# Kernel optimization log

Hardware: AMD Instinct MI355X
Metric: run time of the kernel (lower is better)

Reference implementation:

```python
import jax, jax.numpy as jnp
import numpy as np

B, S, HID, HEADS = 1, 2048, 4096, 32
HEAD_D = HID // HEADS
SCALE = float(1.0 / np.sqrt(HEAD_D))  # = 1/norm_factor^2 with use_mup=False


def setup_inputs() -> dict:
    key = jax.random.key(0)
    k0, k1, k2, k3, k4 = jax.random.split(key, 5)
    return {
        "x": jax.random.normal(k0, (B, S, HID), jnp.float32),
        "attn_qkvw": jax.random.normal(k1, (HID, 3 * HID), jnp.float32) * 0.02,
        "attn_qkvb": jax.random.normal(k2, (3 * HID,), jnp.float32) * 0.02,
        "attn_ow": jax.random.normal(k3, (HID, HID), jnp.float32) * 0.02,
        "attn_ob": jax.random.normal(k4, (HID,), jnp.float32) * 0.02,
    }


def reference(x, attn_qkvw, attn_qkvb, attn_ow, attn_ob):
    # QKV projection (LinearOp): [B,S,HID] @ [HID,3*HID] + bias -> packed qkv
    qkv = x @ attn_qkvw + attn_qkvb
    q, k, v = jnp.split(qkv, 3, axis=-1)  # each [B,S,HID]

    def to_heads(t):
        return t.reshape(B, S, HEADS, HEAD_D)

    q, k, v = to_heads(q), to_heads(k), to_heads(v)
    # flash kernel math: softmax(scale * q k^T + causal mask) @ v (numerically
    # stable online softmax == standard stable softmax)
    scores = jnp.einsum("bqhd,bkhd->bhqk", q, k) * jnp.float32(SCALE)
    causal = jnp.tril(jnp.ones((S, S), dtype=bool))  # P_SEQ = 0
    scores = jnp.where(causal[None, None], scores, jnp.float32(-jnp.inf))
    attn = jax.nn.softmax(scores, axis=-1)
    ctx = jnp.einsum("bhqk,bkhd->bqhd", attn, v).reshape(B, S, HID)
    # output projection
    return ctx @ attn_ow + attn_ob
```

## Files before the change

### kernel.cpp

```cpp
#include <hip/hip_runtime.h>
#include <hip/hip_bf16.h>
#include <math.h>

typedef __bf16 bf16_t;
typedef __bf16 bf16x8 __attribute__((ext_vector_type(8)));
typedef float f32x4 __attribute__((ext_vector_type(4)));

#define AS1 __attribute__((address_space(1)))
#define AS3 __attribute__((address_space(3)))

static constexpr int S_  = 2048;
static constexpr int HID = 4096;
static constexpr int NH  = 32;
static constexpr int HD  = 128;
static constexpr int N3  = 3 * HID;
static constexpr float SCALE = 0.08838834764831845f;

__global__ void cvt_f32_bf16(const float* __restrict__ in, bf16_t* __restrict__ out, int n4) {
  int i = blockIdx.x * blockDim.x + threadIdx.x;
  if (i >= n4) return;
  float4 v = ((const float4*)in)[i];
  union { bf16_t h[4]; short4 s4; } u;
  u.h[0] = (bf16_t)v.x; u.h[1] = (bf16_t)v.y; u.h[2] = (bf16_t)v.z; u.h[3] = (bf16_t)v.w;
  ((short4*)out)[i] = u.s4;
}

__global__ __launch_bounds__(256) void transcvt64(
    const float* __restrict__ in, bf16_t* __restrict__ out, int R, int C) {
  __shared__ float t[64][65];
  const int r0 = blockIdx.y * 64, c0 = blockIdx.x * 64;
  const int tid = threadIdx.x;
  const int rr = tid >> 4, c4 = (tid & 15) * 4;
#pragma unroll
  for (int it = 0; it < 4; ++it) {
    float4 v = *(const float4*)&in[(size_t)(r0 + rr + it * 16) * C + c0 + c4];
    t[rr + it * 16][c4 + 0] = v.x;
    t[rr + it * 16][c4 + 1] = v.y;
    t[rr + it * 16][c4 + 2] = v.z;
    t[rr + it * 16][c4 + 3] = v.w;
  }
  __syncthreads();
  const int cc = tid >> 3, r8 = (tid & 7) * 8;
#pragma unroll
  for (int it = 0; it < 2; ++it) {
    const int c = cc + it * 32;
    bf16x8 w;
#pragma unroll
    for (int j = 0; j < 8; ++j) w[j] = (bf16_t)t[r8 + j][c];
    *(bf16x8*)&out[(size_t)(c0 + c) * R + r0 + r8] = w;
  }
}

__global__ void vtrans(const bf16_t* __restrict__ qkv, bf16_t* __restrict__ vt) {
  __shared__ bf16_t t[32][33];
  int h = blockIdx.z;
  int s0 = blockIdx.x * 32, d0 = blockIdx.y * 32;
  int tx = threadIdx.x, ty = threadIdx.y;
#pragma unroll
  for (int i = 0; i < 32; i += 8)
    t[ty + i][tx] = qkv[(size_t)(s0 + ty + i) * N3 + 2 * HID + h * HD + d0 + tx];
  __syncthreads();
#pragma unroll
  for (int i = 0; i < 32; i += 8)
    vt[(size_t)(h * HD + d0 + ty + i) * S_ + s0 + tx] = t[tx][ty + i];
}

template <bool STG, int VMC>
__device__ __forceinline__ void wstep(
    const char* slot, int aoff, int boff,
    const bf16_t* gA, const bf16_t* gB, int kst, size_t row64,
    char* stgA, char* stgB, f32x4 (&acc)[8][4]) {
  bf16x8 a[8], b[4];
#pragma unroll
  for (int mi = 0; mi < 8; ++mi) a[mi] = *(const bf16x8*)(slot + aoff + mi * 1024);
#pragma unroll
  for (int ni = 0; ni < 4; ++ni) b[ni] = *(const bf16x8*)(slot + 16384 + boff + ni * 1024);
  if constexpr (STG) {
#pragma unroll
    for (int i = 0; i < 4; ++i)
      __builtin_amdgcn_global_load_lds((const AS1 void*)(gA + i * row64 + kst),
                                       (AS3 void*)(stgA + i * 4096), 16, 0, 0);
#pragma unroll
    for (int j = 0; j < 2; ++j)
      __builtin_amdgcn_global_load_lds((const AS1 void*)(gB + j * row64 + kst),
                                       (AS3 void*)(stgB + j * 4096), 16, 0, 0);
  }
  if constexpr (VMC == 6)      asm volatile("s_waitcnt vmcnt(6)" ::: "memory");
  else if constexpr (VMC == 0) asm volatile("s_waitcnt vmcnt(0)" ::: "memory");
  asm volatile("s_waitcnt lgkmcnt(0)" ::: "memory");
  __builtin_amdgcn_s_barrier();
  __builtin_amdgcn_s_setprio(1);
#pragma unroll
  for (int mi = 0; mi < 8; ++mi)
#pragma unroll
    for (int ni = 0; ni < 4; ++ni)
      acc[mi][ni] = __builtin_amdgcn_mfma_f32_16x16x32_bf16(a[mi], b[ni], acc[mi][ni], 0, 0, 0);
  __builtin_amdgcn_s_setprio(0);
}

__global__ __launch_bounds__(256, 2) void gemm_w(
    const bf16_t* __restrict__ A, const bf16_t* __restrict__ BT,
    const float* __restrict__ bias, bf16_t* __restrict__ C,
    int M, int N, int K, int ntiles) {
  extern __shared__ char smem[];
  const int tid = threadIdx.x;
  const int wv = tid >> 6, ln = tid & 63;
  const int lr = ln & 15, lg = ln >> 4;
  const int wm = wv >> 1, wn = wv & 1;

  const int nx = N >> 7;
  const int chunk = ntiles >> 3;

  const int lrow = wv * 16 + (ln >> 2);
  const int lcol = ((ln & 3) << 3) ^ ((ln & 32) >> 1);
  const size_t row64 = (size_t)64 * K;
  const int sw = (lr & 8) << 2;
  const int aoff = (wm * 128 + lr) * 64 + ((lg * 16) ^ sw);
  const int boff = (wn * 64 + lr) * 64 + ((lg * 16) ^ sw);
  const int NT = K >> 5;

  for (int tt = blockIdx.x; tt < ntiles; tt += gridDim.x) {
    const int wg = (tt & 7) * chunk + (tt >> 3);
    const int m0 = (wg / nx) * 256, n0 = (wg % nx) * 128;

    const bf16_t* gA = A + (size_t)(m0 + lrow) * K + lcol;
    const bf16_t* gB = BT + (size_t)(n0 + lrow) * K + lcol;

    f32x4 acc[8][4] = {};

#pragma unroll
    for (int t = 0; t < 2; ++t) {
      char* dA = smem + t * 24576 + wv * 1024;
      char* dB = dA + 16384;
#pragma unroll
      for (int i = 0; i < 4; ++i)
        __builtin_amdgcn_global_load_lds((const AS1 void*)(gA + i * row64 + t * 32),
                                         (AS3 void*)(dA + i * 4096), 16, 0, 0);
#pragma unroll
      for (int j = 0; j < 2; ++j)
        __builtin_amdgcn_global_load_lds((const AS1 void*)(gB + j * row64 + t * 32),
                                         (AS3 void*)(dB + j * 4096), 16, 0, 0);
    }
    asm volatile("s_waitcnt vmcnt(6)" ::: "memory");
    __builtin_amdgcn_s_barrier();

    int slot = 0, nslot = 2;
    int t = 0;
    for (; t < NT - 2; ++t) {
      char* sb = smem + nslot * 24576 + wv * 1024;
      wstep<true, 6>(smem + slot * 24576, aoff, boff, gA, gB, (t + 2) * 32,
                     row64, sb, sb + 16384, acc);
      slot = (slot == 2) ? 0 : slot + 1;
      nslot = (nslot == 2) ? 0 : nslot + 1;
    }
    wstep<false, 0>(smem + slot * 24576, aoff, boff, gA, gB, 0, row64, smem, smem, acc);
    slot = (slot == 2) ? 0 : slot + 1;
    wstep<false, -1>(smem + slot * 24576, aoff, boff, gA, gB, 0, row64, smem, smem, acc);

#pragma unroll
    for (int mi = 0; mi < 8; ++mi)
#pragma unroll
      for (int ni = 0; ni < 4; ++ni) {
        const int col = n0 + wn * 64 + ni * 16 + lr;
        const float bv = bias[col];
#pragma unroll
        for (int i = 0; i < 4; ++i) {
          const int row = m0 + wm * 128 + mi * 16 + lg * 4 + i;
          C[(size_t)row * N + col] = (bf16_t)(acc[mi][ni][i] + bv);
        }
      }
  }
}

template <bool STG, int VMC>
__device__ __forceinline__ void tile_step(
    const char* slot, int aoff, int boff,
    const bf16_t* gA, const bf16_t* gB, int kst, size_t skA,
    char* stg_dst, f32x4 (&acc)[4][4]) {
  bf16x8 a[4], b[4];
#pragma unroll
  for (int mi = 0; mi < 4; ++mi) a[mi] = *(const bf16x8*)(slot + aoff + mi * 1024);
#pragma unroll
  for (int ni = 0; ni < 4; ++ni) b[ni] = *(const bf16x8*)(slot + 16384 + boff + ni * 1024);
  if constexpr (STG) {
    __builtin_amdgcn_global_load_lds((const AS1 void*)(gA + kst), (AS3 void*)(stg_dst), 16, 0, 0);
    __builtin_amdgcn_global_load_lds((const AS1 void*)(gA + skA + kst), (AS3 void*)(stg_dst + 8192), 16, 0, 0);
    __builtin_amdgcn_global_load_lds((const AS1 void*)(gB + kst), (AS3 void*)(stg_dst + 16384), 16, 0, 0);
  }
  if constexpr (VMC == 3)      asm volatile("s_waitcnt vmcnt(3)" ::: "memory");
  else if constexpr (VMC == 0) asm volatile("s_waitcnt vmcnt(0)" ::: "memory");
  asm volatile("s_waitcnt lgkmcnt(0)" ::: "memory");
  __builtin_amdgcn_s_barrier();
  __builtin_amdgcn_s_setprio(1);
#pragma unroll
  for (int mi = 0; mi < 4; ++mi)
#pragma unroll
    for (int ni = 0; ni < 4; ++ni)
      acc[mi][ni] = __builtin_amdgcn_mfma_f32_16x16x32_bf16(a[mi], b[ni], acc[mi][ni], 0, 0, 0);
  __builtin_amdgcn_s_setprio(0);
}

template <typename OutT>
__global__ __launch_bounds__(512, 4) void gemm_p(
    const bf16_t* __restrict__ A, const bf16_t* __restrict__ BT,
    const float* __restrict__ bias, OutT* __restrict__ C,
    int M, int N, int K, int ntiles) {
  extern __shared__ char smem[];
  const int tid = threadIdx.x;
  const int wv = tid >> 6, ln = tid & 63;
  const int lr = ln & 15, lg = ln >> 4;
  const int wm = wv >> 1, wn = wv & 1;

  const int nx = N >> 7;
  const int chunk = ntiles >> 3;

  const int lrow = wv * 16 + (ln >> 2);
  const int lcol = ((ln & 3) << 3) ^ ((ln & 32) >> 1);
  const size_t skA = (size_t)128 * K;
  const int sw = (lr & 8) << 2;
  const int aoff = (wm * 64 + lr) * 64 + ((lg * 16) ^ sw);
  const int boff = (wn * 64 + lr) * 64 + ((lg * 16) ^ sw);
  const int NT = K >> 5;

  for (int tt = blockIdx.x; tt < ntiles; tt += gridDim.x) {
    const int wg = (tt & 7) * chunk + (tt >> 3);
    const int m0 = (wg / nx) * 256, n0 = (wg % nx) * 128;

    const bf16_t* gA = A + (size_t)(m0 + lrow) * K + lcol;
    const bf16_t* gB = BT + (size_t)(n0 + lrow) * K + lcol;

    f32x4 acc[4][4] = {};

#pragma unroll
    for (int t = 0; t < 2; ++t) {
      char* d = smem + t * 24576 + wv * 1024;
      __builtin_amdgcn_global_load_lds((const AS1 void*)(gA + t * 32), (AS3 void*)(d), 16, 0, 0);
      __builtin_amdgcn_global_load_lds((const AS1 void*)(gA + skA + t * 32), (AS3 void*)(d + 8192), 16, 0, 0);
      __builtin_amdgcn_global_load_lds((const AS1 void*)(gB + t * 32), (AS3 void*)(d + 16384), 16, 0, 0);
    }
    asm volatile("s_waitcnt vmcnt(3)" ::: "memory");
    __builtin_amdgcn_s_barrier();

    int slot = 0, nslot = 2;
    int t = 0;
    for (; t < NT - 2; ++t) {
      tile_step<true, 3>(smem + slot * 24576, aoff, boff, gA, gB, (t + 2) * 32,
                         skA, smem + nslot * 24576 + wv * 1024, acc);
      slot = (slot == 2) ? 0 : slot + 1;
      nslot = (nslot == 2) ? 0 : nslot + 1;
    }
    tile_step<false, 0>(smem + slot * 24576, aoff, boff, gA, gB, 0, skA, smem, acc);
    slot = (slot == 2) ? 0 : slot + 1;
    tile_step<false, -1>(smem + slot * 24576, aoff, boff, gA, gB, 0, skA, smem, acc);

#pragma unroll
    for (int mi = 0; mi < 4; ++mi)
#pragma unroll
      for (int ni = 0; ni < 4; ++ni) {
        const int col = n0 + wn * 64 + ni * 16 + lr;
        const float bv = bias[col];
#pragma unroll
        for (int i = 0; i < 4; ++i) {
          const int row = m0 + wm * 64 + mi * 16 + lg * 4 + i;
          C[(size_t)row * N + col] = (OutT)(acc[mi][ni][i] + bv);
        }
      }
  }
}

__global__ __launch_bounds__(256, 2) void attn_fwd(
    const bf16_t* __restrict__ qkv, const bf16_t* __restrict__ vt,
    bf16_t* __restrict__ ctx) {
  __shared__ __align__(16) bf16_t Ks[64][136];
  __shared__ __align__(16) bf16_t Vts[128][72];

  const int tid = threadIdx.x;
  const int wv = tid >> 6, ln = tid & 63;
  bf16_t* Pl = &Ks[0][0] + wv * (32 * 68);

  const int bid = blockIdx.x;
  const int a = bid >> 3;
  const int hsub = a >> 4;
  const int h  = ((bid & 7) << 2) + hsub;
  const int qt = 15 - (((a & 15) + (hsub << 2)) & 15);
  const int q0 = qt * 128;
  const int lr = ln & 15, lg = ln >> 4;
  const int rbase = q0 + 32 * wv;

  bf16x8 qf[2][4];
#pragma unroll
  for (int rg = 0; rg < 2; ++rg)
#pragma unroll
    for (int kk = 0; kk < 4; ++kk) {
      bf16x8 r = *(const bf16x8*)(qkv + (size_t)(rbase + 16 * rg + lr) * N3 + h * HD + kk * 32 + lg * 8);
#pragma unroll
      for (int j = 0; j < 8; ++j) r[j] = (bf16_t)((float)r[j] * SCALE);
      qf[rg][kk] = r;
    }

  f32x4 oacc[2][8] = {};
  float mrow[2][4], psum[2][4];
#pragma unroll
  for (int rg = 0; rg < 2; ++rg)
#pragma unroll
    for (int i = 0; i < 4; ++i) { mrow[rg][i] = -INFINITY; psum[rg][i] = 0.f; }

  const int ntiles = 2 * qt + 2;
  for (int t = 0; t < ntiles; ++t) {
    const int kv0 = t * 64;
    __syncthreads();
#pragma unroll
    for (int it = 0; it < 4; ++it) {
      int c = tid + it * 256;
      {
        int row = c >> 4, col = (c & 15) * 8;
        *(bf16x8*)&Ks[row][col] =
            *(const bf16x8*)(qkv + (size_t)(kv0 + row) * N3 + HID + h * HD + col);
      }
      {
        int row = c >> 3, col = (c & 7) * 8;
        *(bf16x8*)&Vts[row][col] =
            *(const bf16x8*)(vt + (size_t)(h * HD + row) * S_ + kv0 + col);
      }
    }
    __syncthreads();

    f32x4 sacc[2][4] = {};
#pragma unroll
    for (int kk = 0; kk < 4; ++kk)
#pragma unroll
      for (int ni = 0; ni < 4; ++ni) {
        bf16x8 kf = *(const bf16x8*)&Ks[16 * ni + lr][kk * 32 + lg * 8];
        sacc[0][ni] = __builtin_amdgcn_mfma_f32_16x16x32_bf16(qf[0][kk], kf, sacc[0][ni], 0, 0, 0);
        sacc[1][ni] = __builtin_amdgcn_mfma_f32_16x16x32_bf16(qf[1][kk], kf, sacc[1][ni], 0, 0, 0);
      }

    float p[2][4][4];
    float mx[2][4];
    bool grow = false;
#pragma unroll
    for (int rg = 0; rg < 2; ++rg) {
      const bool needmask = (kv0 + 63 > rbase + 16 * rg);
#pragma unroll
      for (int i = 0; i < 4; ++i) {
        const int row = rbase + 16 * rg + lg * 4 + i;
        float m_ = -INFINITY;
#pragma unroll
        for (int ni = 0; ni < 4; ++ni) {
          float s = sacc[rg][ni][i];
          if (needmask && (kv0 + 16 * ni + lr > row)) s = -INFINITY;
          p[rg][ni][i] = s;
          m_ = fmaxf(m_, s);
        }
        m_ = fmaxf(m_, __shfl_xor(m_, 1, 64));
        m_ = fmaxf(m_, __shfl_xor(m_, 2, 64));
        m_ = fmaxf(m_, __shfl_xor(m_, 4, 64));
        m_ = fmaxf(m_, __shfl_xor(m_, 8, 64));
        mx[rg][i] = m_;
        grow |= (m_ > mrow[rg][i]);
      }
    }
    if (__any(grow)) {
#pragma unroll
      for (int rg = 0; rg < 2; ++rg) {
        float alpha[4];
#pragma unroll
        for (int i = 0; i < 4; ++i) {
          const float mn = fmaxf(mrow[rg][i], mx[rg][i]);
          alpha[i] = __expf(mrow[rg][i] - mn);
          mrow[rg][i] = mn;
          psum[rg][i] *= alpha[i];
        }
#pragma unroll
        for (int nf = 0; nf < 8; ++nf)
#pragma unroll
          for (int i = 0; i < 4; ++i) oacc[rg][nf][i] *= alpha[i];
      }
    }
#pragma unroll
    for (int rg = 0; rg < 2; ++rg)
#pragma unroll
      for (int i = 0; i < 4; ++i) {
        float ps = 0.f;
#pragma unroll
        for (int ni = 0; ni < 4; ++ni) {
          float e = __expf(p[rg][ni][i] - mrow[rg][i]);
          p[rg][ni][i] = e;
          ps += e;
        }
        psum[rg][i] += ps;
      }

    __syncthreads();

#pragma unroll
    for (int rg = 0; rg < 2; ++rg)
#pragma unroll
      for (int ni = 0; ni < 4; ++ni)
#pragma unroll
        for (int i = 0; i < 4; ++i)
          Pl[(16 * rg + lg * 4 + i) * 68 + 16 * ni + lr] = (bf16_t)p[rg][ni][i];

#pragma unroll
    for (int kk2 = 0; kk2 < 2; ++kk2) {
      bf16x8 pf0 = *(const bf16x8*)&Pl[lr * 68 + kk2 * 32 + lg * 8];
      bf16x8 pf1 = *(const bf16x8*)&Pl[(16 + lr) * 68 + kk2 * 32 + lg * 8];
#pragma unroll
      for (int nf = 0; nf < 8; ++nf) {
        bf16x8 vf = *(const bf16x8*)&Vts[16 * nf + lr][kk2 * 32 + lg * 8];
        oacc[0][nf] = __builtin_amdgcn_mfma_f32_16x16x32_bf16(pf0, vf, oacc[0][nf], 0, 0, 0);
        oacc[1][nf] = __builtin_amdgcn_mfma_f32_16x16x32_bf16(pf1, vf, oacc[1][nf], 0, 0, 0);
      }
    }
  }

#pragma unroll
  for (int rg = 0; rg < 2; ++rg) {
#pragma unroll
    for (int i = 0; i < 4; ++i) {
      float s = psum[rg][i];
      s += __shfl_xor(s, 1, 64);
      s += __shfl_xor(s, 2, 64);
      s += __shfl_xor(s, 4, 64);
      s += __shfl_xor(s, 8, 64);
      psum[rg][i] = 1.f / s;
    }
#pragma unroll
    for (int nf = 0; nf < 8; ++nf)
#pragma unroll
      for (int i = 0; i < 4; ++i) {
        int row = rbase + 16 * rg + lg * 4 + i;
        int col = h * HD + 16 * nf + lr;
        ctx[(size_t)row * HID + col] = (bf16_t)(oacc[rg][nf][i] * psum[rg][i]);
      }
  }
}

extern "C" void kernel_launch(void* const* d_in, const int* in_sizes, int n_in,
                              void* d_out, int out_size, void* d_ws, size_t ws_size,
                              hipStream_t stream) {
  const float* x    = (const float*)d_in[0];
  const float* wqkv = (const float*)d_in[1];
  const float* bqkv = (const float*)d_in[2];
  const float* ow   = (const float*)d_in[3];
  const float* ob   = (const float*)d_in[4];
  float* out = (float*)d_out;

  char* w = (char*)d_ws;
  bf16_t* xb    = (bf16_t*)(w);
  bf16_t* wqkvT = (bf16_t*)(w + (size_t)16777216);
  bf16_t* qkv   = (bf16_t*)(w + (size_t)117440512);
  bf16_t* vt    = (bf16_t*)(w + (size_t)167772160);
  bf16_t* ctx   = (bf16_t*)(w + (size_t)184549376);
  bf16_t* owT   = (bf16_t*)(w + (size_t)201326592);

  (void)in_sizes; (void)n_in; (void)out_size; (void)ws_size;

  cvt_f32_bf16<<<(S_ * HID / 4 + 255) / 256, 256, 0, stream>>>(x, xb, S_ * HID / 4);
  transcvt64<<<dim3(N3 / 64, HID / 64), 256, 0, stream>>>(wqkv, wqkvT, HID, N3);
  transcvt64<<<dim3(HID / 64, HID / 64), 256, 0, stream>>>(ow, owT, HID, HID);
  gemm_w<<<512, 256, 73728, stream>>>(xb, wqkvT, bqkv, qkv, S_, N3, HID,
                                      (S_ / 256) * (N3 / 128));
  vtrans<<<dim3(S_ / 32, HD / 32, NH), dim3(32, 8), 0, stream>>>(qkv, vt);
  attn_fwd<<<(S_ / 128) * NH, 256, 0, stream>>>(qkv, vt, ctx);
  gemm_p<float><<<256, 512, 73728, stream>>>(ctx, owT, ob, out, S_, HID, HID,
                                             (S_ / 256) * (HID / 128));
}
```

Before: 503.9 us.

## Restructure QKV GEMM to 2 waves with 128x128 per-wave tiles and register double-buffering

The QKV projection GEMM now uses 128-thread blocks (2 waves) where each wave computes a 128x128 output sub-tile (8x8 MFMA fragments) instead of 4 waves with 128x64 each. LDS fragments for the next k-step are loaded into a second register set while MFMAs run on the current one, with a sched_barrier to keep the ordering. The goal is a higher MFMA-to-LDS-read ratio and hiding LDS latency behind compute. In exchange it uses far more VGPRs/AGPRs (256 accumulators plus 32 fragment vectors) and runs fewer waves per CU, which lowers occupancy and latency hiding for the global loads.

```diff
diff --git a/kernel.cpp b/kernel.cpp
--- a/kernel.cpp
+++ b/kernel.cpp
@@ -65,40 +65,50 @@
     vt[(size_t)(h * HD + d0 + ty + i) * S_ + s0 + tx] = t[tx][ty + i];
 }
 
-template <bool STG, int VMC>
-__device__ __forceinline__ void wstep(
-    const char* slot, int aoff, int boff,
-    const bf16_t* gA, const bf16_t* gB, int kst, size_t row64,
-    char* stgA, char* stgB, f32x4 (&acc)[8][4]) {
-  bf16x8 a[8], b[4];
-#pragma unroll
-  for (int mi = 0; mi < 8; ++mi) a[mi] = *(const bf16x8*)(slot + aoff + mi * 1024);
-#pragma unroll
-  for (int ni = 0; ni < 4; ++ni) b[ni] = *(const bf16x8*)(slot + 16384 + boff + ni * 1024);
-  if constexpr (STG) {
-#pragma unroll
-    for (int i = 0; i < 4; ++i)
-      __builtin_amdgcn_global_load_lds((const AS1 void*)(gA + i * row64 + kst),
-                                       (AS3 void*)(stgA + i * 4096), 16, 0, 0);
-#pragma unroll
-    for (int j = 0; j < 2; ++j)
-      __builtin_amdgcn_global_load_lds((const AS1 void*)(gB + j * row64 + kst),
-                                       (AS3 void*)(stgB + j * 4096), 16, 0, 0);
-  }
-  if constexpr (VMC == 6)      asm volatile("s_waitcnt vmcnt(6)" ::: "memory");
-  else if constexpr (VMC == 0) asm volatile("s_waitcnt vmcnt(0)" ::: "memory");
+__device__ __forceinline__ f32x4 MFMA(bf16x8 a, bf16x8 b, f32x4 c) {
+  return __builtin_amdgcn_mfma_f32_16x16x32_bf16(a, b, c, 0, 0, 0);
+}
+
+template <int MODE>
+__device__ __forceinline__ void wstep2(
+    const char* slotNext, int aoff, int boff,
+    const bf16_t* gA, const bf16_t* gB, int kst, size_t s32,
+    char* stgA, char* stgB,
+    bf16x8 (&cur)[16], bf16x8 (&nxt)[16], f32x4 (&acc)[8][8]) {
+  if constexpr (MODE == 0) {
+#pragma unroll
+    for (int i = 0; i < 8; ++i)
+      __builtin_amdgcn_global_load_lds((const AS1 void*)(gA + i * s32 + kst),
+                                       (AS3 void*)(stgA + i * 2048), 16, 0, 0);
+#pragma unroll
+    for (int j = 0; j < 4; ++j)
+      __builtin_amdgcn_global_load_lds((const AS1 void*)(gB + j * s32 + kst),
+                                       (AS3 void*)(stgB + j * 2048), 16, 0, 0);
+    asm volatile("s_waitcnt vmcnt(12)" ::: "memory");
+  } else if constexpr (MODE == 1) {
+    asm volatile("s_waitcnt vmcnt(0)" ::: "memory");
+  }
   asm volatile("s_waitcnt lgkmcnt(0)" ::: "memory");
   __builtin_amdgcn_s_barrier();
+  __builtin_amdgcn_sched_barrier(0);
+  if constexpr (MODE != 2) {
+#pragma unroll
+    for (int mi = 0; mi < 8; ++mi)
+      nxt[mi] = *(const bf16x8*)(slotNext + aoff + mi * 1024);
+#pragma unroll
+    for (int ni = 0; ni < 8; ++ni)
+      nxt[8 + ni] = *(const bf16x8*)(slotNext + 16384 + boff + ni * 1024);
+  }
   __builtin_amdgcn_s_setprio(1);
 #pragma unroll
   for (int mi = 0; mi < 8; ++mi)
 #pragma unroll
-    for (int ni = 0; ni < 4; ++ni)
-      acc[mi][ni] = __builtin_amdgcn_mfma_f32_16x16x32_bf16(a[mi], b[ni], acc[mi][ni], 0, 0, 0);
+    for (int ni = 0; ni < 8; ++ni)
+      acc[mi][ni] = MFMA(cur[mi], cur[8 + ni], acc[mi][ni]);
   __builtin_amdgcn_s_setprio(0);
 }
 
-__global__ __launch_bounds__(256, 2) void gemm_w(
+__global__ __launch_bounds__(128, 1) void gemm_w(
     const bf16_t* __restrict__ A, const bf16_t* __restrict__ BT,
     const float* __restrict__ bias, bf16_t* __restrict__ C,
     int M, int N, int K, int ntiles) {
@@ -106,17 +116,16 @@
   const int tid = threadIdx.x;
   const int wv = tid >> 6, ln = tid & 63;
   const int lr = ln & 15, lg = ln >> 4;
-  const int wm = wv >> 1, wn = wv & 1;
 
   const int nx = N >> 7;
   const int chunk = ntiles >> 3;
 
   const int lrow = wv * 16 + (ln >> 2);
   const int lcol = ((ln & 3) << 3) ^ ((ln & 32) >> 1);
-  const size_t row64 = (size_t)64 * K;
+  const size_t s32 = (size_t)32 * K;
   const int sw = (lr & 8) << 2;
-  const int aoff = (wm * 128 + lr) * 64 + ((lg * 16) ^ sw);
-  const int boff = (wn * 64 + lr) * 64 + ((lg * 16) ^ sw);
+  const int aoff = (wv * 128 + lr) * 64 + ((lg * 16) ^ sw);
+  const int boff = lr * 64 + ((lg * 16) ^ sw);
   const int NT = K >> 5;
 
   for (int tt = blockIdx.x; tt < ntiles; tt += gridDim.x) {
@@ -126,46 +135,61 @@
     const bf16_t* gA = A + (size_t)(m0 + lrow) * K + lcol;
     const bf16_t* gB = BT + (size_t)(n0 + lrow) * K + lcol;
 
-    f32x4 acc[8][4] = {};
+    f32x4 acc[8][8] = {};
+    bf16x8 rA[16], rB[16];
 
 #pragma unroll
     for (int t = 0; t < 2; ++t) {
       char* dA = smem + t * 24576 + wv * 1024;
       char* dB = dA + 16384;
 #pragma unroll
-      for (int i = 0; i < 4; ++i)
-        __builtin_amdgcn_global_load_lds((const AS1 void*)(gA + i * row64 + t * 32),
-                                         (AS3 void*)(dA + i * 4096), 16, 0, 0);
-#pragma unroll
-      for (int j = 0; j < 2; ++j)
-        __builtin_amdgcn_global_load_lds((const AS1 void*)(gB + j * row64 + t * 32),
-                                         (AS3 void*)(dB + j * 4096), 16, 0, 0);
-    }
-    asm volatile("s_waitcnt vmcnt(6)" ::: "memory");
+      for (int i = 0; i < 8; ++i)
+        __builtin_amdgcn_global_load_lds((const AS1 void*)(gA + i * s32 + t * 32),
+                                         (AS3 void*)(dA + i * 2048), 16, 0, 0);
+#pragma unroll
+      for (int j = 0; j < 4; ++j)
+        __builtin_amdgcn_global_load_lds((const AS1 void*)(gB + j * s32 + t * 32),
+                                         (AS3 void*)(dB + j * 2048), 16, 0, 0);
+    }
+    asm volatile("s_waitcnt vmcnt(12)" ::: "memory");
     __builtin_amdgcn_s_barrier();
-
-    int slot = 0, nslot = 2;
-    int t = 0;
-    for (; t < NT - 2; ++t) {
-      char* sb = smem + nslot * 24576 + wv * 1024;
-      wstep<true, 6>(smem + slot * 24576, aoff, boff, gA, gB, (t + 2) * 32,
-                     row64, sb, sb + 16384, acc);
-      slot = (slot == 2) ? 0 : slot + 1;
-      nslot = (nslot == 2) ? 0 : nslot + 1;
-    }
-    wstep<false, 0>(smem + slot * 24576, aoff, boff, gA, gB, 0, row64, smem, smem, acc);
-    slot = (slot == 2) ? 0 : slot + 1;
-    wstep<false, -1>(smem + slot * 24576, aoff, boff, gA, gB, 0, row64, smem, smem, acc);
+    __builtin_amdgcn_sched_barrier(0);
+#pragma unroll
+    for (int mi = 0; mi < 8; ++mi) rA[mi] = *(const bf16x8*)(smem + aoff + mi * 1024);
+#pragma unroll
+    for (int ni = 0; ni < 8; ++ni) rA[8 + ni] = *(const bf16x8*)(smem + 16384 + boff + ni * 1024);
+
+    int sc = 0;
+    for (int t = 0; t < NT - 2; t += 2) {
+      int s1 = sc + 1; if (s1 > 2) s1 -= 3;
+      int s2 = sc + 2; if (s2 > 2) s2 -= 3;
+      {
+        char* sg = smem + s2 * 24576 + wv * 1024;
+        wstep2<0>(smem + s1 * 24576, aoff, boff, gA, gB, (t + 2) * 32, s32,
+                  sg, sg + 16384, rA, rB, acc);
+      }
+      {
+        char* sg = smem + sc * 24576 + wv * 1024;
+        wstep2<0>(smem + s2 * 24576, aoff, boff, gA, gB, (t + 3) * 32, s32,
+                  sg, sg + 16384, rB, rA, acc);
+      }
+      sc = s2;
+    }
+    {
+      int s1 = sc + 1; if (s1 > 2) s1 -= 3;
+      wstep2<1>(smem + s1 * 24576, aoff, boff, gA, gB, 0, s32, smem, smem, rA, rB, acc);
+    }
+    wstep2<2>(smem, aoff, boff, gA, gB, 0, s32, smem, smem, rB, rA, acc);
 
 #pragma unroll
     for (int mi = 0; mi < 8; ++mi)
 #pragma unroll
-      for (int ni = 0; ni < 4; ++ni) {
-        const int col = n0 + wn * 64 + ni * 16 + lr;
+      for (int ni = 0; ni < 8; ++ni) {
+        const int col = n0 + ni * 16 + lr;
         const float bv = bias[col];
 #pragma unroll
         for (int i = 0; i < 4; ++i) {
-          const int row = m0 + wm * 128 + mi * 16 + lg * 4 + i;
+          const int row = m0 + wv * 128 + mi * 16 + lg * 4 + i;
           C[(size_t)row * N + col] = (bf16_t)(acc[mi][ni][i] + bv);
         }
       }
@@ -459,7 +483,7 @@
   cvt_f32_bf16<<<(S_ * HID / 4 + 255) / 256, 256, 0, stream>>>(x, xb, S_ * HID / 4);
   transcvt64<<<dim3(N3 / 64, HID / 64), 256, 0, stream>>>(wqkv, wqkvT, HID, N3);
   transcvt64<<<dim3(HID / 64, HID / 64), 256, 0, stream>>>(ow, owT, HID, HID);
-  gemm_w<<<512, 256, 73728, stream>>>(xb, wqkvT, bqkv, qkv, S_, N3, HID,
+  gemm_w<<<512, 128, 73728, stream>>>(xb, wqkvT, bqkv, qkv, S_, N3, HID,
                                       (S_ / 256) * (N3 / 128));
   vtrans<<<dim3(S_ / 32, HD / 32, NH), dim3(32, 8), 0, stream>>>(qkv, vt);
   attn_fwd<<<(S_ / 128) * NH, 256, 0, stream>>>(qkv, vt, ctx);
```

Result: slower. 544.2 us (+8.0%).
